# Performance work log

Hardware: AMD Instinct MI355X
Metric: run time of the kernel (lower is better)

## Reference

```python
import jax, jax.numpy as jnp
import numpy as np

B, L = 4, 1024
D_IN, D_MODEL, DEPTH = 8, 512, 4
D_INNER, D_STATE, D_CONV = 2 * D_MODEL, 16, 4
DT_RANK = (D_MODEL + 15) // 16  # 32


def setup_inputs():
    key = jax.random.key(0)
    ks = jax.random.split(key, 12)
    s = 0.02
    inp = {
        "x": jax.random.normal(ks[0], (B, L, D_IN), jnp.float32),
        "in_w": jax.random.normal(ks[1], (D_MODEL, D_IN), jnp.float32) * s,
        "in_b": jnp.zeros((D_MODEL,), jnp.float32),
        "W_xz": jax.random.normal(ks[2], (DEPTH, 2 * D_INNER, D_MODEL), jnp.float32) * s,
        "conv_w": jax.random.normal(ks[3], (DEPTH, D_INNER, D_CONV), jnp.float32) * 0.1,
        "conv_b": jnp.zeros((DEPTH, D_INNER), jnp.float32),
        "W_xp": jax.random.normal(ks[4], (DEPTH, DT_RANK + 2 * D_STATE, D_INNER), jnp.float32) * s,
        "W_dt": jax.random.normal(ks[5], (DEPTH, D_INNER, DT_RANK), jnp.float32) * 0.1,
        "b_dt": jax.random.uniform(ks[6], (DEPTH, D_INNER), jnp.float32, -4.0, -2.0),
        "A_log": jnp.broadcast_to(jnp.log(jnp.arange(1, D_STATE + 1, dtype=jnp.float32)), (DEPTH, D_INNER, D_STATE)) + 0.0,
        "D_param": jnp.ones((DEPTH, D_INNER), jnp.float32),
        "W_out": jax.random.normal(ks[7], (DEPTH, D_MODEL, D_INNER), jnp.float32) * s,
        "ln_g": jnp.ones((D_MODEL,), jnp.float32),
        "ln_b": jnp.zeros((D_MODEL,), jnp.float32),
    }
    return inp


def _silu(x):
    return x * jax.nn.sigmoid(x)


def _mamba_layer(h, Wxz, cw, cb, Wxp, Wdt, bdt, A_log, Dp, Wout):
    # in_proj -> (x, z)
    xz = jnp.einsum('bld,ed->ble', h, Wxz)           # (B,L,2*D_INNER)
    xc, z = jnp.split(xz, 2, axis=-1)
    # causal depthwise conv1d, kernel D_CONV
    xp = jnp.pad(xc, ((0, 0), (D_CONV - 1, 0), (0, 0)))
    xconv = sum(xp[:, k:k + L, :] * cw[:, k] for k in range(D_CONV)) + cb
    u = _silu(xconv)                                 # (B,L,D_INNER)
    # x_proj -> dt, B, C
    xdbl = jnp.einsum('bld,ed->ble', u, Wxp)
    dt_lr = xdbl[..., :DT_RANK]
    Bm = xdbl[..., DT_RANK:DT_RANK + D_STATE]        # (B,L,D_STATE)
    Cm = xdbl[..., DT_RANK + D_STATE:]               # (B,L,D_STATE)
    dt = jax.nn.softplus(jnp.einsum('blr,dr->bld', dt_lr, Wdt) + bdt)  # (B,L,D_INNER)
    A = -jnp.exp(A_log)                              # (D_INNER,D_STATE)

    def step(hst, inp):
        dt_t, B_t, C_t, u_t = inp                    # (B,Di),(B,S),(B,S),(B,Di)
        dA = jnp.exp(dt_t[..., None] * A)            # (B,Di,S)
        dBu = dt_t[..., None] * B_t[:, None, :] * u_t[..., None]
        hst = dA * hst + dBu
        y_t = jnp.einsum('bds,bs->bd', hst, C_t)
        return hst, y_t

    h0 = jnp.zeros((h.shape[0], D_INNER, D_STATE), h.dtype)
    xs = (dt.transpose(1, 0, 2), Bm.transpose(1, 0, 2), Cm.transpose(1, 0, 2), u.transpose(1, 0, 2))
    _, ys = jax.lax.scan(step, h0, xs)
    y = ys.transpose(1, 0, 2) + u * Dp               # (B,L,D_INNER)
    y = y * _silu(z)
    return jnp.einsum('ble,de->bld', y, Wout)


def reference(x, in_w, in_b, W_xz, conv_w, conv_b, W_xp, W_dt, b_dt, A_log, D_param, W_out, ln_g, ln_b):
    h = jnp.einsum('bli,di->bld', x, in_w) + in_b
    for i in range(DEPTH):
        h = _mamba_layer(h, W_xz[i], conv_w[i], conv_b[i], W_xp[i], W_dt[i], b_dt[i], A_log[i], D_param[i], W_out[i])
    mu = h.mean(-1, keepdims=True)
    var = ((h - mu) ** 2).mean(-1, keepdims=True)
    return (h - mu) * jax.lax.rsqrt(var + 1e-5) * ln_g + ln_b
```

## Files before the change

### kernel.cpp

```cpp
#include <hip/hip_runtime.h>
#include <math.h>

#define B_      4
#define L_      1024
#define D_INNC  8
#define DMODEL  512
#define DEPTH_  4
#define DINNER  1024
#define DSTATE  16
#define DCONV   4
#define DTRANK  32
#define MTOT    (B_*L_)
#define CHUNKS  64
#define CLEN    16
#define XPSPLIT 8

typedef float f32x4 __attribute__((ext_vector_type(4)));
typedef short s16x8 __attribute__((ext_vector_type(8)));
typedef unsigned short u16;
typedef unsigned short u16x4v __attribute__((ext_vector_type(4)));

#define GLOBAL_AS __attribute__((address_space(1)))
#define LDS_AS    __attribute__((address_space(3)))

__device__ __forceinline__ u16 f2bf(float v) {
    unsigned b = __float_as_uint(v);
    return (u16)((b + 0x7FFF + ((b >> 16) & 1)) >> 16);
}
__device__ __forceinline__ float bf2f(u16 h) {
    return __uint_as_float((unsigned)h << 16);
}

__global__ __launch_bounds__(256) void in_proj_kernel(
    const float* __restrict__ x, const float* __restrict__ w,
    const float* __restrict__ bias, u16* __restrict__ hb)
{
    int idx = blockIdx.x * 256 + threadIdx.x;
    int m = idx / DMODEL, d = idx % DMODEL;
    const float* xr = x + m * D_INNC;
    const float* wr = w + d * D_INNC;
    float acc = bias[d];
#pragma unroll
    for (int k = 0; k < D_INNC; ++k) acc += xr[k] * wr[k];
    hb[idx] = f2bf(acc);
}

__global__ __launch_bounds__(256) void wconv_kernel(
    const float* __restrict__ W, u16* __restrict__ Wb)
{
    int i = blockIdx.x * 256 + threadIdx.x;
    const float* src = W + (size_t)i * 8;
    float4 f0 = *(const float4*)src;
    float4 f1 = *(const float4*)(src + 4);
    float f[8] = {f0.x,f0.y,f0.z,f0.w,f1.x,f1.y,f1.z,f1.w};
    s16x8 hv;
#pragma unroll
    for (int e = 0; e < 8; ++e) hv[e] = (short)f2bf(f[e]);
    *(s16x8*)(Wb + (size_t)i * 8) = hv;
}

template<int ROWS>
__device__ __forceinline__ void stage_tile(
    const u16* __restrict__ src, int ld, int koff, u16* lds, int t)
{
    const int l = t & 63, w = t >> 6;
    const int r_in = l >> 2, s = l & 3;
#pragma unroll
    for (int p = 0; p < ROWS / 64; ++p) {
        int rb = (p * 4 + w) * 16;
        int r  = rb + r_in;
        int sw = s ^ ((r ^ (r >> 2)) & 3);
        const u16* g = src + (size_t)r * ld + koff + sw * 8;
        u16* lp = lds + rb * 32;
        __builtin_amdgcn_global_load_lds(
            (const GLOBAL_AS void*)g, (LDS_AS void*)lp, 16, 0, 0);
    }
}

template<int BM, int BN, int MODE>
__global__ __launch_bounds__(256, 2) void gemm_bf16(
    const u16* __restrict__ A, int lda,
    const u16* __restrict__ B, int ldb,
    void* __restrict__ C0, void* __restrict__ C1,
    int ldc, int K)
{
    constexpr int FM = BM / 32;
    constexpr int FN = BN / 32;
    __shared__ __align__(16) u16 As[2][BM * 32];
    __shared__ __align__(16) u16 Bs[2][BN * 32];

    const int t    = threadIdx.x;
    const int lane = t & 63;
    const int w    = t >> 6;
    const int wm   = (w >> 1) * (BM / 2);
    const int wn   = (w & 1) * (BN / 2);
    const int quad = lane >> 4;
    const int l16  = lane & 15;
    const int m0   = blockIdx.y * BM;
    const int n0   = (MODE == 6) ? 0 : blockIdx.x * BN;
    const int kbase= (MODE == 6) ? blockIdx.x * K : 0;
    const int sq   = (quad ^ ((l16 ^ (l16 >> 2)) & 3)) * 8;

    const u16* Abase = A + (size_t)m0 * lda;
    const u16* Bbase = B + (size_t)n0 * ldb;

    f32x4 acc[FM][FN];
#pragma unroll
    for (int i = 0; i < FM; ++i)
#pragma unroll
        for (int j = 0; j < FN; ++j) acc[i][j] = (f32x4){0.f,0.f,0.f,0.f};

    stage_tile<BM>(Abase, lda, kbase, As[0], t);
    stage_tile<BN>(Bbase, ldb, kbase, Bs[0], t);

    int cur = 0;
    for (int kk = 0; kk < K; kk += 32) {
        __syncthreads();
        int kn = kk + 32;
        if (kn < K) {
            stage_tile<BM>(Abase, lda, kbase + kn, As[cur ^ 1], t);
            stage_tile<BN>(Bbase, ldb, kbase + kn, Bs[cur ^ 1], t);
        }
        s16x8 afr[FM], bfr[FN];
#pragma unroll
        for (int i = 0; i < FM; ++i) {
            int row = wm + i * 16 + l16;
            afr[i] = *(const s16x8*)&As[cur][row * 32 + sq];
        }
#pragma unroll
        for (int j = 0; j < FN; ++j) {
            int row = wn + j * 16 + l16;
            bfr[j] = *(const s16x8*)&Bs[cur][row * 32 + sq];
        }
#pragma unroll
        for (int i = 0; i < FM; ++i)
#pragma unroll
            for (int j = 0; j < FN; ++j)
                acc[i][j] = __builtin_amdgcn_mfma_f32_16x16x32_bf16(afr[i], bfr[j], acc[i][j], 0, 0, 0);
        cur ^= 1;
    }

    if constexpr (MODE == 2) {
        u16* C = (u16*)C0;
#pragma unroll
        for (int i = 0; i < FM; ++i)
#pragma unroll
            for (int j = 0; j < FN; ++j) {
                int col = n0 + wn + j*16 + l16;
#pragma unroll
                for (int r = 0; r < 4; ++r) {
                    int row = m0 + wm + i*16 + quad*4 + r;
                    C[(size_t)row * ldc + col] = f2bf(acc[i][j][r]);
                }
            }
    } else if constexpr (MODE == 6) {
        float* P = (float*)C0 + (size_t)blockIdx.x * MTOT * 64;
#pragma unroll
        for (int i = 0; i < FM; ++i)
#pragma unroll
            for (int j = 0; j < FN; ++j) {
                int col = wn + j*16 + l16;
#pragma unroll
                for (int r = 0; r < 4; ++r) {
                    int row = m0 + wm + i*16 + quad*4 + r;
                    P[(size_t)row * 64 + col] = acc[i][j][r];
                }
            }
    } else if constexpr (MODE == 4) {
        u16* dtb_ = (u16*)C0;
        const float* bdt = (const float*)C1;
#pragma unroll
        for (int i = 0; i < FM; ++i)
#pragma unroll
            for (int j = 0; j < FN; ++j) {
                int col = n0 + wn + j*16 + l16;
                float bb = bdt[col];
#pragma unroll
                for (int r = 0; r < 4; ++r) {
                    int row = m0 + wm + i*16 + quad*4 + r;
                    float v = acc[i][j][r] + bb;
                    float sp = (v > 20.f) ? v : log1pf(__expf(v));
                    dtb_[(size_t)row * ldc + col] = f2bf(sp);
                }
            }
    } else {
        u16* xcb = (u16*)C0;
        u16* szb = (u16*)C1;
#pragma unroll
        for (int i = 0; i < FM; ++i)
#pragma unroll
            for (int j = 0; j < FN; ++j) {
                int col = n0 + wn + j*16 + l16;
                bool isz = col >= DINNER;
                int cc = col & (DINNER - 1);
                u16* dst = isz ? szb : xcb;
#pragma unroll
                for (int r = 0; r < 4; ++r) {
                    int row = m0 + wm + i*16 + quad*4 + r;
                    float v = acc[i][j][r];
                    if (isz) v = v / (1.f + __expf(-v));
                    dst[(size_t)row * DINNER + cc] = f2bf(v);
                }
            }
    }
}

__global__ __launch_bounds__(256) void xpred_kernel(
    const float* __restrict__ part, u16* __restrict__ dtlr,
    float* __restrict__ xd)
{
    int tid = blockIdx.x * 256 + threadIdx.x;
    int m = tid >> 4, c4 = (tid & 15) * 4;
    float s0 = 0.f, s1 = 0.f, s2 = 0.f, s3 = 0.f;
#pragma unroll
    for (int p = 0; p < XPSPLIT; ++p) {
        float4 v = *(const float4*)&part[((size_t)p * MTOT + m) * 64 + c4];
        s0 += v.x; s1 += v.y; s2 += v.z; s3 += v.w;
    }
    if (c4 < 32) {
        u16x4v o;
        o[0] = f2bf(s0); o[1] = f2bf(s1); o[2] = f2bf(s2); o[3] = f2bf(s3);
        *(u16x4v*)&dtlr[(size_t)m * 32 + c4] = o;
    } else {
        float4 o; o.x = s0; o.y = s1; o.z = s2; o.w = s3;
        *(float4*)&xd[(size_t)m * 64 + c4] = o;
    }
}

__global__ __launch_bounds__(256) void conv_silu_kernel(
    const u16* __restrict__ xcb, const float* __restrict__ cw,
    const float* __restrict__ cb, u16* __restrict__ ub)
{
    int idx = (blockIdx.x * 256 + threadIdx.x) * 2;
    int m = idx >> 10;
    int d = idx & (DINNER - 1);
    int l = m & (L_ - 1);

    const float4 w0 = *(const float4*)&cw[d * 4];
    const float4 w1 = *(const float4*)&cw[(d + 1) * 4];
    float a0 = cb[d], a1 = cb[d + 1];
#pragma unroll
    for (int k = 0; k < 4; ++k) {
        int lag = 3 - k;
        if (l >= lag) {
            unsigned v = *(const unsigned*)&xcb[(size_t)(m - lag) * DINNER + d];
            float x0 = bf2f((u16)(v & 0xffff));
            float x1 = bf2f((u16)(v >> 16));
            float wk0 = (&w0.x)[k], wk1 = (&w1.x)[k];
            a0 += x0 * wk0; a1 += x1 * wk1;
        }
    }
    a0 = a0 / (1.f + __expf(-a0));
    a1 = a1 / (1.f + __expf(-a1));
    unsigned pack = (unsigned)f2bf(a0) | ((unsigned)f2bf(a1) << 16);
    *(unsigned*)&ub[idx] = pack;
}

__global__ __launch_bounds__(256) void scan1_kernel(
    const u16* __restrict__ ub, const float* xdbl,
    const u16* __restrict__ dtb, const float* __restrict__ A_log,
    u16* __restrict__ hfinal, float* __restrict__ dsum)
{
    __shared__ float Bs[CLEN][16];
    const int blk  = blockIdx.x;
    const int dblk = blk & 3;
    const int c    = (blk >> 2) & (CHUNKS - 1);
    const int b    = blk >> 8;
    const int d    = dblk * 256 + threadIdx.x;
    const int mbase = b * L_ + c * CLEN;

    {
        int idx = threadIdx.x;
        int tt = idx >> 4, ss = idx & 15;
        Bs[tt][ss] = xdbl[(size_t)(mbase + tt) * 64 + 32 + ss];
    }
    float A[16];
    {
        float4 a4[4];
#pragma unroll
        for (int q = 0; q < 4; ++q) a4[q] = *(const float4*)&A_log[d * 16 + q * 4];
        const float* af = (const float*)a4;
#pragma unroll
        for (int s = 0; s < 16; ++s) A[s] = -__expf(af[s]);
    }
    __syncthreads();

    float h[16];
#pragma unroll
    for (int s = 0; s < 16; ++s) h[s] = 0.f;
    float dts = 0.f;

    for (int t0 = 0; t0 < CLEN; t0 += 8) {
        float dt8[8], u8[8];
#pragma unroll
        for (int j = 0; j < 8; ++j) {
            int m = mbase + t0 + j;
            dt8[j] = bf2f(dtb[(size_t)m * DINNER + d]);
            u8[j]  = bf2f(ub [(size_t)m * DINNER + d]);
        }
#pragma unroll
        for (int j = 0; j < 8; ++j) {
            float dtv = dt8[j], dtu = dtv * u8[j];
            dts += dtv;
            float Bt[16];
#pragma unroll
            for (int q = 0; q < 4; ++q)
                *(float4*)&Bt[q*4] = *(const float4*)&Bs[t0 + j][q*4];
#pragma unroll
            for (int s = 0; s < 16; ++s) {
                float dA = __expf(dtv * A[s]);
                h[s] = dA * h[s] + dtu * Bt[s];
            }
        }
    }
    size_t base = ((size_t)(b * CHUNKS + c) * DINNER + d) * 16;
    s16x8 p0, p1;
#pragma unroll
    for (int s = 0; s < 8; ++s) { p0[s] = (short)f2bf(h[s]); p1[s] = (short)f2bf(h[s+8]); }
    *(s16x8*)&hfinal[base]     = p0;
    *(s16x8*)&hfinal[base + 8] = p1;
    dsum[(size_t)(b * CHUNKS + c) * DINNER + d] = dts;
}

__global__ __launch_bounds__(256) void scan2_kernel(
    u16* __restrict__ hfinal, const float* __restrict__ dsum,
    const float* __restrict__ A_log)
{
    int t = blockIdx.x * 256 + threadIdx.x;
    int s = t & 15, d = (t >> 4) & (DINNER - 1), b = t >> 14;
    float As = -__expf(A_log[d * DSTATE + s]);
    float h = 0.f;
    for (int c0 = 0; c0 < CHUNKS; c0 += 8) {
        float hf8[8], dts8[8];
#pragma unroll
        for (int j = 0; j < 8; ++j) {
            int c = c0 + j;
            size_t i = (size_t)(b * CHUNKS + c) * DINNER + d;
            dts8[j] = dsum[i];
            hf8[j]  = bf2f(hfinal[i * 16 + s]);
        }
#pragma unroll
        for (int j = 0; j < 8; ++j) {
            int c = c0 + j;
            size_t idx = ((size_t)(b * CHUNKS + c) * DINNER + d) * 16 + s;
            hfinal[idx] = f2bf(h);
            h = __expf(As * dts8[j]) * h + hf8[j];
        }
    }
}

__global__ __launch_bounds__(256) void scan3_kernel(
    const u16* __restrict__ szb, const u16* __restrict__ ub,
    const float* xdbl, const u16* __restrict__ dtb,
    const float* __restrict__ A_log, const float* __restrict__ Dp,
    const u16* __restrict__ hstart, u16* __restrict__ yb)
{
    __shared__ float Bs[CLEN][16];
    __shared__ float Cs[CLEN][16];
    const int blk  = blockIdx.x;
    const int dblk = blk & 3;
    const int c    = (blk >> 2) & (CHUNKS - 1);
    const int b    = blk >> 8;
    const int d    = dblk * 256 + threadIdx.x;
    const int mbase = b * L_ + c * CLEN;

    {
        int idx = threadIdx.x;
        int tt = idx >> 4, ss = idx & 15;
        Bs[tt][ss] = xdbl[(size_t)(mbase + tt) * 64 + 32 + ss];
        Cs[tt][ss] = xdbl[(size_t)(mbase + tt) * 64 + 48 + ss];
    }
    float A[16];
    {
        float4 a4[4];
#pragma unroll
        for (int q = 0; q < 4; ++q) a4[q] = *(const float4*)&A_log[d * 16 + q * 4];
        const float* af = (const float*)a4;
#pragma unroll
        for (int s = 0; s < 16; ++s) A[s] = -__expf(af[s]);
    }
    const float Dval = Dp[d];

    float h[16];
    {
        size_t base = ((size_t)(b * CHUNKS + c) * DINNER + d) * 16;
        s16x8 p0 = *(const s16x8*)&hstart[base];
        s16x8 p1 = *(const s16x8*)&hstart[base + 8];
#pragma unroll
        for (int s = 0; s < 8; ++s) { h[s] = bf2f((u16)p0[s]); h[s+8] = bf2f((u16)p1[s]); }
    }
    __syncthreads();

    for (int t0 = 0; t0 < CLEN; t0 += 8) {
        float dt8[8], u8[8], sz8[8];
#pragma unroll
        for (int j = 0; j < 8; ++j) {
            int m = mbase + t0 + j;
            dt8[j] = bf2f(dtb[(size_t)m * DINNER + d]);
            u8[j]  = bf2f(ub [(size_t)m * DINNER + d]);
            sz8[j] = bf2f(szb[(size_t)m * DINNER + d]);
        }
#pragma unroll
        for (int j = 0; j < 8; ++j) {
            float dtv = dt8[j], dtu = dtv * u8[j];
            float Bt[16], Ct[16];
#pragma unroll
            for (int q = 0; q < 4; ++q) {
                *(float4*)&Bt[q*4] = *(const float4*)&Bs[t0 + j][q*4];
                *(float4*)&Ct[q*4] = *(const float4*)&Cs[t0 + j][q*4];
            }
            float yv = 0.f;
#pragma unroll
            for (int s = 0; s < 16; ++s) {
                float dA = __expf(dtv * A[s]);
                h[s] = dA * h[s] + dtu * Bt[s];
                yv += h[s] * Ct[s];
            }
            int m = mbase + t0 + j;
            yb[(size_t)m * DINNER + d] = f2bf((yv + u8[j] * Dval) * sz8[j]);
        }
    }
}

__global__ __launch_bounds__(256) void ln_kernel(
    const u16* __restrict__ hb, const float* __restrict__ g,
    const float* __restrict__ bta, float* __restrict__ out)
{
    int m = blockIdx.x;
    size_t base = (size_t)m * DMODEL;
    int t = threadIdx.x;
    float v0 = bf2f(hb[base + t]);
    float v1 = bf2f(hb[base + t + 256]);
    float sum = v0 + v1, sq = v0*v0 + v1*v1;
#pragma unroll
    for (int off = 32; off; off >>= 1) {
        sum += __shfl_down(sum, off);
        sq  += __shfl_down(sq,  off);
    }
    __shared__ float ls[4], lq[4];
    int w = t >> 6;
    if ((t & 63) == 0) { ls[w] = sum; lq[w] = sq; }
    __syncthreads();
    sum = ls[0] + ls[1] + ls[2] + ls[3];
    sq  = lq[0] + lq[1] + lq[2] + lq[3];
    float mu  = sum * (1.f / DMODEL);
    float var = sq * (1.f / DMODEL) - mu * mu;
    float rs  = rsqrtf(var + 1e-5f);
    out[base + t]       = (v0 - mu) * rs * g[t]       + bta[t];
    out[base + t + 256] = (v1 - mu) * rs * g[t + 256] + bta[t + 256];
}

extern "C" void kernel_launch(void* const* d_in, const int* in_sizes, int n_in,
                              void* d_out, int out_size, void* d_ws, size_t ws_size,
                              hipStream_t stream)
{
    const float* x      = (const float*)d_in[0];
    const float* in_w   = (const float*)d_in[1];
    const float* in_b   = (const float*)d_in[2];
    const float* W_xz   = (const float*)d_in[3];
    const float* conv_w = (const float*)d_in[4];
    const float* conv_b = (const float*)d_in[5];
    const float* W_xp   = (const float*)d_in[6];
    const float* W_dt   = (const float*)d_in[7];
    const float* b_dt   = (const float*)d_in[8];
    const float* A_log  = (const float*)d_in[9];
    const float* D_par  = (const float*)d_in[10];
    const float* W_out  = (const float*)d_in[11];
    const float* ln_g   = (const float*)d_in[12];
    const float* ln_b   = (const float*)d_in[13];
    float* out = (float*)d_out;

    float* ws      = (float*)d_ws;
    float* hbF     = ws;
    float* hfinF   = hbF    + 1048576;
    float* xcbF    = hfinF  + 2097152;
    float* szbF    = xcbF   + 2097152;
    float* ubF     = szbF   + 2097152;
    float* xdbl    = ubF    + 2097152;
    float* dtbF    = xdbl   + 262144;
    float* ybF     = dtbF   + 2097152;
    float* wxzF    = ybF    + 2097152;
    float* woutF   = wxzF   + 2097152;
    float* wxpF    = woutF  + 1048576;
    float* wdtF    = wxpF   + 131072;
    float* dsum    = wdtF   + 65536;
    float* dtlrF   = dsum   + 262144;
    float* xpart   = dtlrF  + 65536;

    u16* hb     = (u16*)hbF;
    u16* hfinal = (u16*)hfinF;
    u16* xcb  = (u16*)xcbF;
    u16* szb  = (u16*)szbF;
    u16* ub   = (u16*)ubF;
    u16* dtb  = (u16*)dtbF;
    u16* yb   = (u16*)ybF;
    u16* wxzb  = (u16*)wxzF;
    u16* woutb = (u16*)woutF;
    u16* wxpb  = (u16*)wxpF;
    u16* wdtb  = (u16*)wdtF;
    u16* dtlrb = (u16*)dtlrF;

    wconv_kernel<<<(DEPTH_*2048*DMODEL/8)/256, 256, 0, stream>>>(W_xz, wxzb);
    wconv_kernel<<<(DEPTH_*DMODEL*DINNER/8)/256, 256, 0, stream>>>(W_out, woutb);
    wconv_kernel<<<(DEPTH_*64*DINNER/8)/256, 256, 0, stream>>>(W_xp, wxpb);
    wconv_kernel<<<(DEPTH_*DINNER*DTRANK/8)/256, 256, 0, stream>>>(W_dt, wdtb);

    in_proj_kernel<<<MTOT*DMODEL/256, 256, 0, stream>>>(x, in_w, in_b, hb);

    for (int layer = 0; layer < DEPTH_; ++layer) {
        const float* cw    = conv_w + (size_t)layer * DINNER * DCONV;
        const float* cb    = conv_b + (size_t)layer * DINNER;
        const float* bdt   = b_dt   + (size_t)layer * DINNER;
        const float* Alog  = A_log  + (size_t)layer * DINNER * DSTATE;
        const float* Dp    = D_par  + (size_t)layer * DINNER;
        const u16* wxzL    = wxzb  + (size_t)layer * 2048 * DMODEL;
        const u16* woutL   = woutb + (size_t)layer * DMODEL * DINNER;
        const u16* wxpL    = wxpb  + (size_t)layer * 64 * DINNER;
        const u16* wdtL    = wdtb  + (size_t)layer * DINNER * DTRANK;

        gemm_bf16<128,128,1><<<dim3(2048/128, MTOT/128), 256, 0, stream>>>(
            hb, DMODEL, wxzL, DMODEL, xcb, szb, 0, DMODEL);
        conv_silu_kernel<<<MTOT*DINNER/2/256, 256, 0, stream>>>(xcb, cw, cb, ub);
        gemm_bf16<64,64,6><<<dim3(XPSPLIT, MTOT/64), 256, 0, stream>>>(
            ub, DINNER, wxpL, DINNER, xpart, nullptr, 0, DINNER/XPSPLIT);
        xpred_kernel<<<MTOT*16/256, 256, 0, stream>>>(xpart, dtlrb, xdbl);
        gemm_bf16<64,64,4><<<dim3(DINNER/64, MTOT/64), 256, 0, stream>>>(
            dtlrb, DTRANK, wdtL, DTRANK, dtb, (void*)bdt, DINNER, DTRANK);
        scan1_kernel<<<B_*CHUNKS*(DINNER/256), 256, 0, stream>>>(ub, xdbl, dtb, Alog, hfinal, dsum);
        scan2_kernel<<<(B_*DINNER*DSTATE)/256, 256, 0, stream>>>(hfinal, dsum, Alog);
        scan3_kernel<<<B_*CHUNKS*(DINNER/256), 256, 0, stream>>>(szb, ub, xdbl, dtb, Alog, Dp, hfinal, yb);
        gemm_bf16<64,64,2><<<dim3(DMODEL/64, MTOT/64), 256, 0, stream>>>(
            yb, DINNER, woutL, DINNER, hb, nullptr, DMODEL, DINNER);
    }

    ln_kernel<<<MTOT, 256, 0, stream>>>(hb, ln_g, ln_b, out);
}
```

Measured before the change: 598.8 us.

## Fuse split-K reduction and dt projection into scan kernels, merge weight conversion

Removes the xpred reduction kernel and the dt-projection GEMM by having scan1 and scan3 each sum the x_proj split-K partials into shared memory and compute dt = softplus(W_dt·dt_lr + b) per thread in registers. This avoids writing and reading the full-size bf16 dt tensor and saves two launches per layer. It also merges the four weight-conversion launches into one. In exchange, the dt computation and the partial-sum reads are done twice, once in scan1 and once in scan3, and register pressure in the scan kernels rises.

```diff
diff --git a/kernel.cpp b/kernel.cpp
--- a/kernel.cpp
+++ b/kernel.cpp
@@ -45,18 +45,26 @@
     hb[idx] = f2bf(acc);
 }
 
-__global__ __launch_bounds__(256) void wconv_kernel(
-    const float* __restrict__ W, u16* __restrict__ Wb)
+__global__ __launch_bounds__(256) void wprep_kernel(
+    const float* __restrict__ Wxz, const float* __restrict__ Wout,
+    const float* __restrict__ Wxp, const float* __restrict__ Wdt,
+    u16* __restrict__ wxzb, u16* __restrict__ woutb,
+    u16* __restrict__ wxpb, u16* __restrict__ wdtb)
 {
     int i = blockIdx.x * 256 + threadIdx.x;
-    const float* src = W + (size_t)i * 8;
-    float4 f0 = *(const float4*)src;
-    float4 f1 = *(const float4*)(src + 4);
+    const float* src; u16* dst; int off;
+    if (i < 524288)      { src = Wxz;  dst = wxzb;  off = i; }
+    else if (i < 786432) { src = Wout; dst = woutb; off = i - 524288; }
+    else if (i < 819200) { src = Wxp;  dst = wxpb;  off = i - 786432; }
+    else                 { src = Wdt;  dst = wdtb;  off = i - 819200; }
+    const float* s = src + (size_t)off * 8;
+    float4 f0 = *(const float4*)s;
+    float4 f1 = *(const float4*)(s + 4);
     float f[8] = {f0.x,f0.y,f0.z,f0.w,f1.x,f1.y,f1.z,f1.w};
     s16x8 hv;
 #pragma unroll
     for (int e = 0; e < 8; ++e) hv[e] = (short)f2bf(f[e]);
-    *(s16x8*)(Wb + (size_t)i * 8) = hv;
+    *(s16x8*)(dst + (size_t)off * 8) = hv;
 }
 
 template<int ROWS>
@@ -166,23 +174,6 @@
                     P[(size_t)row * 64 + col] = acc[i][j][r];
                 }
             }
-    } else if constexpr (MODE == 4) {
-        u16* dtb_ = (u16*)C0;
-        const float* bdt = (const float*)C1;
-#pragma unroll
-        for (int i = 0; i < FM; ++i)
-#pragma unroll
-            for (int j = 0; j < FN; ++j) {
-                int col = n0 + wn + j*16 + l16;
-                float bb = bdt[col];
-#pragma unroll
-                for (int r = 0; r < 4; ++r) {
-                    int row = m0 + wm + i*16 + quad*4 + r;
-                    float v = acc[i][j][r] + bb;
-                    float sp = (v > 20.f) ? v : log1pf(__expf(v));
-                    dtb_[(size_t)row * ldc + col] = f2bf(sp);
-                }
-            }
     } else {
         u16* xcb = (u16*)C0;
         u16* szb = (u16*)C1;
@@ -202,28 +193,6 @@
                     dst[(size_t)row * DINNER + cc] = f2bf(v);
                 }
             }
-    }
-}
-
-__global__ __launch_bounds__(256) void xpred_kernel(
-    const float* __restrict__ part, u16* __restrict__ dtlr,
-    float* __restrict__ xd)
-{
-    int tid = blockIdx.x * 256 + threadIdx.x;
-    int m = tid >> 4, c4 = (tid & 15) * 4;
-    float s0 = 0.f, s1 = 0.f, s2 = 0.f, s3 = 0.f;
-#pragma unroll
-    for (int p = 0; p < XPSPLIT; ++p) {
-        float4 v = *(const float4*)&part[((size_t)p * MTOT + m) * 64 + c4];
-        s0 += v.x; s1 += v.y; s2 += v.z; s3 += v.w;
-    }
-    if (c4 < 32) {
-        u16x4v o;
-        o[0] = f2bf(s0); o[1] = f2bf(s1); o[2] = f2bf(s2); o[3] = f2bf(s3);
-        *(u16x4v*)&dtlr[(size_t)m * 32 + c4] = o;
-    } else {
-        float4 o; o.x = s0; o.y = s1; o.z = s2; o.w = s3;
-        *(float4*)&xd[(size_t)m * 64 + c4] = o;
     }
 }
 
@@ -256,12 +225,55 @@
     *(unsigned*)&ub[idx] = pack;
 }
 
+__device__ __forceinline__ void sum_partials(
+    const float* __restrict__ xpart, int mbase, float xs[CLEN][64], int tid)
+{
+    int idx4 = tid * 4;
+    int row = idx4 >> 6, col = idx4 & 63;
+    float4 s = (float4){0.f, 0.f, 0.f, 0.f};
+#pragma unroll
+    for (int p = 0; p < XPSPLIT; ++p) {
+        float4 v = *(const float4*)&xpart[((size_t)p * MTOT + mbase + row) * 64 + col];
+        s.x += v.x; s.y += v.y; s.z += v.z; s.w += v.w;
+    }
+    *(float4*)&xs[row][col] = s;
+}
+
+__device__ __forceinline__ void compute_dt(
+    const float xs[CLEN][64], const u16* __restrict__ wdtL,
+    const float* __restrict__ bdt, int d, float dtv[CLEN])
+{
+    float wf[32];
+    {
+        const u16* wrow = wdtL + (size_t)d * DTRANK;
+        s16x8 w4[4];
+#pragma unroll
+        for (int q = 0; q < 4; ++q) w4[q] = *(const s16x8*)(wrow + q * 8);
+#pragma unroll
+        for (int q = 0; q < 4; ++q)
+#pragma unroll
+            for (int e = 0; e < 8; ++e) wf[q*8+e] = bf2f((u16)w4[q][e]);
+    }
+    const float bb = bdt[d];
+#pragma unroll
+    for (int m = 0; m < CLEN; ++m) {
+        float a0 = bb;
+#pragma unroll
+        for (int q = 0; q < 8; ++q) {
+            float4 xv = *(const float4*)&xs[m][q*4];
+            a0 += xv.x*wf[q*4] + xv.y*wf[q*4+1] + xv.z*wf[q*4+2] + xv.w*wf[q*4+3];
+        }
+        dtv[m] = (a0 > 20.f) ? a0 : log1pf(__expf(a0));
+    }
+}
+
 __global__ __launch_bounds__(256) void scan1_kernel(
-    const u16* __restrict__ ub, const float* xdbl,
-    const u16* __restrict__ dtb, const float* __restrict__ A_log,
+    const u16* __restrict__ ub, const float* __restrict__ xpart,
+    const u16* __restrict__ wdtL, const float* __restrict__ bdt,
+    const float* __restrict__ A_log,
     u16* __restrict__ hfinal, float* __restrict__ dsum)
 {
-    __shared__ float Bs[CLEN][16];
+    __shared__ float xs[CLEN][64];
     const int blk  = blockIdx.x;
     const int dblk = blk & 3;
     const int c    = (blk >> 2) & (CHUNKS - 1);
@@ -269,11 +281,7 @@
     const int d    = dblk * 256 + threadIdx.x;
     const int mbase = b * L_ + c * CLEN;
 
-    {
-        int idx = threadIdx.x;
-        int tt = idx >> 4, ss = idx & 15;
-        Bs[tt][ss] = xdbl[(size_t)(mbase + tt) * 64 + 32 + ss];
-    }
+    sum_partials(xpart, mbase, xs, threadIdx.x);
     float A[16];
     {
         float4 a4[4];
@@ -285,30 +293,31 @@
     }
     __syncthreads();
 
+    float dtv[CLEN];
+    compute_dt(xs, wdtL, bdt, d, dtv);
+
     float h[16];
 #pragma unroll
     for (int s = 0; s < 16; ++s) h[s] = 0.f;
     float dts = 0.f;
 
+#pragma unroll
     for (int t0 = 0; t0 < CLEN; t0 += 8) {
-        float dt8[8], u8[8];
+        float u8[8];
+#pragma unroll
+        for (int j = 0; j < 8; ++j)
+            u8[j] = bf2f(ub[(size_t)(mbase + t0 + j) * DINNER + d]);
 #pragma unroll
         for (int j = 0; j < 8; ++j) {
-            int m = mbase + t0 + j;
-            dt8[j] = bf2f(dtb[(size_t)m * DINNER + d]);
-            u8[j]  = bf2f(ub [(size_t)m * DINNER + d]);
-        }
-#pragma unroll
-        for (int j = 0; j < 8; ++j) {
-            float dtv = dt8[j], dtu = dtv * u8[j];
-            dts += dtv;
+            float dtvj = dtv[t0 + j], dtu = dtvj * u8[j];
+            dts += dtvj;
             float Bt[16];
 #pragma unroll
             for (int q = 0; q < 4; ++q)
-                *(float4*)&Bt[q*4] = *(const float4*)&Bs[t0 + j][q*4];
+                *(float4*)&Bt[q*4] = *(const float4*)&xs[t0 + j][32 + q*4];
 #pragma unroll
             for (int s = 0; s < 16; ++s) {
-                float dA = __expf(dtv * A[s]);
+                float dA = __expf(dtvj * A[s]);
                 h[s] = dA * h[s] + dtu * Bt[s];
             }
         }
@@ -351,12 +360,12 @@
 
 __global__ __launch_bounds__(256) void scan3_kernel(
     const u16* __restrict__ szb, const u16* __restrict__ ub,
-    const float* xdbl, const u16* __restrict__ dtb,
+    const float* __restrict__ xpart,
+    const u16* __restrict__ wdtL, const float* __restrict__ bdt,
     const float* __restrict__ A_log, const float* __restrict__ Dp,
     const u16* __restrict__ hstart, u16* __restrict__ yb)
 {
-    __shared__ float Bs[CLEN][16];
-    __shared__ float Cs[CLEN][16];
+    __shared__ float xs[CLEN][64];
     const int blk  = blockIdx.x;
     const int dblk = blk & 3;
     const int c    = (blk >> 2) & (CHUNKS - 1);
@@ -364,12 +373,7 @@
     const int d    = dblk * 256 + threadIdx.x;
     const int mbase = b * L_ + c * CLEN;
 
-    {
-        int idx = threadIdx.x;
-        int tt = idx >> 4, ss = idx & 15;
-        Bs[tt][ss] = xdbl[(size_t)(mbase + tt) * 64 + 32 + ss];
-        Cs[tt][ss] = xdbl[(size_t)(mbase + tt) * 64 + 48 + ss];
-    }
+    sum_partials(xpart, mbase, xs, threadIdx.x);
     float A[16];
     {
         float4 a4[4];
@@ -380,6 +384,10 @@
         for (int s = 0; s < 16; ++s) A[s] = -__expf(af[s]);
     }
     const float Dval = Dp[d];
+    __syncthreads();
+
+    float dtv[CLEN];
+    compute_dt(xs, wdtL, bdt, d, dtv);
 
     float h[16];
     {
@@ -389,30 +397,29 @@
 #pragma unroll
         for (int s = 0; s < 8; ++s) { h[s] = bf2f((u16)p0[s]); h[s+8] = bf2f((u16)p1[s]); }
     }
-    __syncthreads();
-
+
+#pragma unroll
     for (int t0 = 0; t0 < CLEN; t0 += 8) {
-        float dt8[8], u8[8], sz8[8];
+        float u8[8], sz8[8];
 #pragma unroll
         for (int j = 0; j < 8; ++j) {
             int m = mbase + t0 + j;
-            dt8[j] = bf2f(dtb[(size_t)m * DINNER + d]);
             u8[j]  = bf2f(ub [(size_t)m * DINNER + d]);
             sz8[j] = bf2f(szb[(size_t)m * DINNER + d]);
         }
 #pragma unroll
         for (int j = 0; j < 8; ++j) {
-            float dtv = dt8[j], dtu = dtv * u8[j];
+            float dtvj = dtv[t0 + j], dtu = dtvj * u8[j];
             float Bt[16], Ct[16];
 #pragma unroll
             for (int q = 0; q < 4; ++q) {
-                *(float4*)&Bt[q*4] = *(const float4*)&Bs[t0 + j][q*4];
-                *(float4*)&Ct[q*4] = *(const float4*)&Cs[t0 + j][q*4];
+                *(float4*)&Bt[q*4] = *(const float4*)&xs[t0 + j][32 + q*4];
+                *(float4*)&Ct[q*4] = *(const float4*)&xs[t0 + j][48 + q*4];
             }
             float yv = 0.f;
 #pragma unroll
             for (int s = 0; s < 16; ++s) {
-                float dA = __expf(dtv * A[s]);
+                float dA = __expf(dtvj * A[s]);
                 h[s] = dA * h[s] + dtu * Bt[s];
                 yv += h[s] * Ct[s];
             }
@@ -476,34 +483,27 @@
     float* xcbF    = hfinF  + 2097152;
     float* szbF    = xcbF   + 2097152;
     float* ubF     = szbF   + 2097152;
-    float* xdbl    = ubF    + 2097152;
-    float* dtbF    = xdbl   + 262144;
-    float* ybF     = dtbF   + 2097152;
+    float* ybF     = ubF    + 2097152;
     float* wxzF    = ybF    + 2097152;
     float* woutF   = wxzF   + 2097152;
     float* wxpF    = woutF  + 1048576;
     float* wdtF    = wxpF   + 131072;
     float* dsum    = wdtF   + 65536;
-    float* dtlrF   = dsum   + 262144;
-    float* xpart   = dtlrF  + 65536;
+    float* xpart   = dsum   + 262144;
 
     u16* hb     = (u16*)hbF;
     u16* hfinal = (u16*)hfinF;
     u16* xcb  = (u16*)xcbF;
     u16* szb  = (u16*)szbF;
     u16* ub   = (u16*)ubF;
-    u16* dtb  = (u16*)dtbF;
     u16* yb   = (u16*)ybF;
     u16* wxzb  = (u16*)wxzF;
     u16* woutb = (u16*)woutF;
     u16* wxpb  = (u16*)wxpF;
     u16* wdtb  = (u16*)wdtF;
-    u16* dtlrb = (u16*)dtlrF;
-
-    wconv_kernel<<<(DEPTH_*2048*DMODEL/8)/256, 256, 0, stream>>>(W_xz, wxzb);
-    wconv_kernel<<<(DEPTH_*DMODEL*DINNER/8)/256, 256, 0, stream>>>(W_out, woutb);
-    wconv_kernel<<<(DEPTH_*64*DINNER/8)/256, 256, 0, stream>>>(W_xp, wxpb);
-    wconv_kernel<<<(DEPTH_*DINNER*DTRANK/8)/256, 256, 0, stream>>>(W_dt, wdtb);
+
+    wprep_kernel<<<3264, 256, 0, stream>>>(W_xz, W_out, W_xp, W_dt,
+                                           wxzb, woutb, wxpb, wdtb);
 
     in_proj_kernel<<<MTOT*DMODEL/256, 256, 0, stream>>>(x, in_w, in_b, hb);
 
@@ -523,12 +523,11 @@
         conv_silu_kernel<<<MTOT*DINNER/2/256, 256, 0, stream>>>(xcb, cw, cb, ub);
         gemm_bf16<64,64,6><<<dim3(XPSPLIT, MTOT/64), 256, 0, stream>>>(
             ub, DINNER, wxpL, DINNER, xpart, nullptr, 0, DINNER/XPSPLIT);
-        xpred_kernel<<<MTOT*16/256, 256, 0, stream>>>(xpart, dtlrb, xdbl);
-        gemm_bf16<64,64,4><<<dim3(DINNER/64, MTOT/64), 256, 0, stream>>>(
-            dtlrb, DTRANK, wdtL, DTRANK, dtb, (void*)bdt, DINNER, DTRANK);
-        scan1_kernel<<<B_*CHUNKS*(DINNER/256), 256, 0, stream>>>(ub, xdbl, dtb, Alog, hfinal, dsum);
+        scan1_kernel<<<B_*CHUNKS*(DINNER/256), 256, 0, stream>>>(
+            ub, xpart, wdtL, bdt, Alog, hfinal, dsum);
         scan2_kernel<<<(B_*DINNER*DSTATE)/256, 256, 0, stream>>>(hfinal, dsum, Alog);
-        scan3_kernel<<<B_*CHUNKS*(DINNER/256), 256, 0, stream>>>(szb, ub, xdbl, dtb, Alog, Dp, hfinal, yb);
+        scan3_kernel<<<B_*CHUNKS*(DINNER/256), 256, 0, stream>>>(
+            szb, ub, xpart, wdtL, bdt, Alog, Dp, hfinal, yb);
         gemm_bf16<64,64,2><<<dim3(DMODEL/64, MTOT/64), 256, 0, stream>>>(
             yb, DINNER, woutL, DINNER, hb, nullptr, DMODEL, DINNER);
     }
```

Result: slower. 645.5 us (+7.8%).
